# Performance work log

Measured on AMD Instinct MI355X. Metric: run time of the kernel, lower is better.

## Reference

```python
import jax, jax.numpy as jnp
import numpy as np

B, D = 16384, 1280      # batch, EfficientNet-b0 feature dim (model._fc.in_features)
C1, C2, C3 = 8, 6, 4    # fanout per tree level: 8 roots, 6 children each, 4 leaves each


def setup_inputs() -> dict:
    key = jax.random.key(0)
    ks = jax.random.split(key, 7)
    sc = 0.02
    x = jax.random.normal(ks[0], (B, D), dtype=jnp.float32)
    # root classifier: self.final = Linear(1280 -> n[0]=8)
    W_final = jax.random.normal(ks[1], (D, C1), dtype=jnp.float32) * sc
    b_final = jnp.zeros((C1,), dtype=jnp.float32)
    # level-1 node linears: Linear(1281 -> 6); split into feature part Wp and upper-scalar column wu
    Wp1 = jax.random.normal(ks[2], (C1, D, C2), dtype=jnp.float32) * sc
    wu1 = jax.random.normal(ks[3], (C1, C2), dtype=jnp.float32) * sc
    b1 = jnp.zeros((C1, C2), dtype=jnp.float32)
    # level-2 node linears: Linear(1281 -> 4)
    Wp2 = jax.random.normal(ks[4], (C1, C2, D, C3), dtype=jnp.float32) * sc
    wu2 = jax.random.normal(ks[5], (C1, C2, C3), dtype=jnp.float32) * sc
    b2 = jnp.zeros((C1, C2, C3), dtype=jnp.float32)
    return {"x": x, "W_final": W_final, "b_final": b_final,
            "Wp1": Wp1, "wu1": wu1, "b1": b1,
            "Wp2": Wp2, "wu2": wu2, "b2": b2}


def reference(x, W_final, b_final, Wp1, wu1, b1, Wp2, wu2, b2):
    # penultimate = x.clone().detach()
    pen = jax.lax.stop_gradient(x)                      # (B, D)
    # root: raw final-linear outputs (NO softmax at root in the torch code)
    u1 = x @ W_final + b_final                          # (B, C1) == upper for level-1 nodes
    # level-1 nodes: line = softmax(Linear([pen, upper_scalar]))
    # Linear([pen, u]) == pen @ Wp + u * wu + b  (batched over all 8 nodes in one GEMM)
    logits1 = jnp.einsum('bd,idc->bic', pen, Wp1) + u1[:, :, None] * wu1[None] + b1[None]
    p1 = jax.nn.softmax(logits1, axis=-1)               # (B, C1, C2)
    u2 = p1 * u1[:, :, None]                            # upper for level-2 nodes
    # level-2 nodes
    logits2 = jnp.einsum('bd,ijdc->bijc', pen, Wp2) + u2[..., None] * wu2[None] + b2[None]
    p2 = jax.nn.softmax(logits2, axis=-1)               # (B, C1, C2, C3)
    u3 = p2 * u2[..., None]                             # upper for leaf nodes
    # output: for each node (sorted by path length, then lexicographic path),
    # the last column of xdict[node] == upper[node]. Row-major reshape matches
    # the sorted key order for single-char labels.
    return jnp.concatenate([u1, u2.reshape(B, C1 * C2), u3.reshape(B, C1 * C2 * C3)], axis=1)
```

## Files before the change

kernel.cpp:

```cpp
#include <hip/hip_runtime.h>
#include <stdint.h>
#include <stddef.h>

#define D_FEAT 1280
#define N_PAD  256
#define N_OUT  248
#define BM     64
#define BK     64
#define K_ITERS 20
#define W_TILE_BYTES (N_PAD * BK * 2)

typedef float f32x4 __attribute__((ext_vector_type(4)));
typedef short s16x8 __attribute__((ext_vector_type(8)));
typedef unsigned int u32x4 __attribute__((ext_vector_type(4)));

__device__ __forceinline__ unsigned short f2bf(float f) {
  union { float f; unsigned int u; } v; v.f = f;
  unsigned int r = (v.u + 0x7fffu + ((v.u >> 16) & 1u)) >> 16;
  return (unsigned short)r;
}

__device__ __forceinline__ unsigned int cvt_pk(float a, float b) {
  unsigned int r;
  asm("v_cvt_pk_bf16_f32 %0, %1, %2" : "=v"(r) : "v"(a), "v"(b));
  return r;
}

__device__ __forceinline__ void gload16(const void* g, void* l) {
  __builtin_amdgcn_global_load_lds(
      (const __attribute__((address_space(1))) void*)g,
      (__attribute__((address_space(3))) void*)l, 16, 0, 0);
}

__global__ __launch_bounds__(256) void pack_w_kernel(
    const float* __restrict__ Wf, const float* __restrict__ Wp1,
    const float* __restrict__ Wp2, unsigned short* __restrict__ out) {
  int chunk = blockIdx.x * 256 + threadIdx.x;
  int s_phys = chunk & 7;
  int n = (chunk >> 3) & 255;
  int kt = chunk >> 11;
  int s_log = s_phys ^ (n & 7);
  int d0 = kt * BK + s_log * 8;
  float v[8];
#pragma unroll
  for (int e = 0; e < 8; ++e) v[e] = 0.0f;
  if (n < 8) {
#pragma unroll
    for (int e = 0; e < 8; ++e) v[e] = Wf[(d0 + e) * 8 + n];
  } else if (n < 56) {
    int m = n - 8;
    const float* base = Wp1 + (size_t)(m / 6) * D_FEAT * 6 + (m % 6);
#pragma unroll
    for (int e = 0; e < 8; ++e) v[e] = base[(d0 + e) * 6];
  } else if (n < 248) {
    int m = n - 56;
    const float* base = Wp2 + ((size_t)(m / 24) * 6 + ((m % 24) >> 2)) * D_FEAT * 4 + (m & 3);
#pragma unroll
    for (int e = 0; e < 8; ++e) v[e] = base[(d0 + e) * 4];
  }
  union { u32x4 u; s16x8 s; } pk;
#pragma unroll
  for (int h = 0; h < 4; ++h) pk.u[h] = cvt_pk(v[2 * h], v[2 * h + 1]);
  *(s16x8*)(out + (size_t)chunk * 8) = pk.s;
}

__global__ __launch_bounds__(512, 2) void tree_head_kernel(
    const float* __restrict__ x, const unsigned short* __restrict__ Wb,
    const float* __restrict__ b_final, const float* __restrict__ wu1,
    const float* __restrict__ b1, const float* __restrict__ wu2,
    const float* __restrict__ b2, float* __restrict__ out) {
  __shared__ __align__(16) char smem[122880];
  char* A0 = smem;
  char* A1 = smem + 8192;
  char* A2 = smem + 16384;
  char* B0 = smem + 24576;
  char* B1 = smem + 57344;
  char* B2 = smem + 90112;

  const int tid  = threadIdx.x;
  const int lane = tid & 63;
  const int wave = tid >> 6;
  const int wm   = wave >> 2;
  const int wn   = wave & 3;
  const int l15  = lane & 15;
  const int lh   = lane >> 4;
  const int row0 = blockIdx.x * BM;

  f32x4 acc[2][4];
#pragma unroll
  for (int m = 0; m < 2; ++m)
#pragma unroll
    for (int n = 0; n < 4; ++n)
#pragma unroll
      for (int j = 0; j < 4; ++j) acc[m][n][j] = 0.0f;

  const int arow = tid >> 3;
  const int aslot = tid & 7;
  const char* aptr = (const char*)x + ((size_t)(row0 + arow) * D_FEAT + aslot * 8) * 4;
  const int awoff = arow * 128 + ((aslot ^ (arow & 7)) << 4);
  const char* bsrc = (const char*)Wb + wave * 1024 + lane * 16;
  const int bdst = wave * 1024;

  f32x4 ra[3][2];

#define STAGEB(kt_, dB_) do {                                                 \
    _Pragma("unroll")                                                         \
    for (int j_ = 0; j_ < 4; ++j_)                                            \
      gload16(bsrc + (size_t)(kt_) * W_TILE_BYTES + j_ * 8192,                \
              (dB_) + bdst + j_ * 8192);                                      \
  } while (0)

#define LOADA(kt_, ri_) do {                                                  \
    ra[ri_][0] = *(const f32x4*)(aptr + (kt_) * 256);                         \
    ra[ri_][1] = *(const f32x4*)(aptr + (kt_) * 256 + 16);                    \
  } while (0)

#define WRITEA(ri_, dA_) do {                                                 \
    union { u32x4 u; s16x8 s; } pk_;                                          \
    pk_.u[0] = cvt_pk(ra[ri_][0][0], ra[ri_][0][1]);                          \
    pk_.u[1] = cvt_pk(ra[ri_][0][2], ra[ri_][0][3]);                          \
    pk_.u[2] = cvt_pk(ra[ri_][1][0], ra[ri_][1][1]);                          \
    pk_.u[3] = cvt_pk(ra[ri_][1][2], ra[ri_][1][3]);                          \
    *(s16x8*)((dA_) + awoff) = pk_.s;                                         \
  } while (0)

#define COMPUTE(cA_, cB_) do {                                                \
    s16x8 fr[2][2];                                                           \
    _Pragma("unroll")                                                         \
    for (int m_ = 0; m_ < 2; ++m_) {                                          \
      int rl_ = wm * 32 + m_ * 16 + l15;                                      \
      _Pragma("unroll")                                                       \
      for (int ks_ = 0; ks_ < 2; ++ks_) {                                     \
        int sl_ = ks_ * 4 + lh;                                               \
        fr[m_][ks_] = *(const s16x8*)((cA_) + rl_ * 128 +                     \
                                      ((sl_ ^ (rl_ & 7)) << 4));              \
      }                                                                       \
    }                                                                         \
    _Pragma("unroll")                                                         \
    for (int ks_ = 0; ks_ < 2; ++ks_) {                                       \
      int sl_ = ks_ * 4 + lh;                                                 \
      _Pragma("unroll")                                                       \
      for (int nf_ = 0; nf_ < 4; ++nf_) {                                     \
        int n_ = wn * 64 + nf_ * 16 + l15;                                    \
        s16x8 b_ = *(const s16x8*)((cB_) + n_ * 128 + ((sl_ ^ (n_ & 7)) << 4));\
        acc[0][nf_] = __builtin_amdgcn_mfma_f32_16x16x32_bf16(fr[0][ks_], b_, acc[0][nf_], 0, 0, 0); \
        acc[1][nf_] = __builtin_amdgcn_mfma_f32_16x16x32_bf16(fr[1][ks_], b_, acc[1][nf_], 0, 0, 0); \
      }                                                                       \
    }                                                                         \
  } while (0)

#define ITER(kt_, cA_, cB_, wA_, sB_, ls_, ws_) do {                          \
    asm volatile("s_waitcnt lgkmcnt(0)" ::: "memory");                        \
    __builtin_amdgcn_sched_barrier(0);                                        \
    __builtin_amdgcn_s_barrier();                                             \
    __builtin_amdgcn_sched_barrier(0);                                        \
    STAGEB((kt_) + 2, sB_);                                                   \
    LOADA((kt_) + 3, ls_);                                                    \
    __builtin_amdgcn_sched_barrier(0);                                        \
    asm volatile("s_waitcnt vmcnt(8)" ::: "memory");                          \
    __builtin_amdgcn_sched_barrier(0);                                        \
    WRITEA(ws_, wA_);                                                         \
    COMPUTE(cA_, cB_);                                                        \
  } while (0)

  STAGEB(0, B0);
  LOADA(0, 0);
  LOADA(1, 1);
  STAGEB(1, B1);
  LOADA(2, 2);
  __builtin_amdgcn_sched_barrier(0);
  asm volatile("s_waitcnt vmcnt(8)" ::: "memory");
  __builtin_amdgcn_sched_barrier(0);
  WRITEA(0, A0);

  for (int t = 0; t < 5; ++t) {
    ITER(3 * t + 0, A0, B0, A1, B2, 0, 1);
    ITER(3 * t + 1, A1, B1, A2, B0, 1, 2);
    ITER(3 * t + 2, A2, B2, A0, B1, 2, 0);
  }
  ITER(15, A0, B0, A1, B2, 0, 1);
  ITER(16, A1, B1, A2, B0, 1, 2);

  asm volatile("s_waitcnt lgkmcnt(0)" ::: "memory");
  __builtin_amdgcn_sched_barrier(0);
  __builtin_amdgcn_s_barrier();
  __builtin_amdgcn_sched_barrier(0);
  STAGEB(19, B1);
  __builtin_amdgcn_sched_barrier(0);
  asm volatile("s_waitcnt vmcnt(6)" ::: "memory");
  __builtin_amdgcn_sched_barrier(0);
  WRITEA(0, A0);
  COMPUTE(A2, B2);

  asm volatile("s_waitcnt lgkmcnt(0)" ::: "memory");
  __builtin_amdgcn_sched_barrier(0);
  __builtin_amdgcn_s_barrier();
  __builtin_amdgcn_sched_barrier(0);
  asm volatile("s_waitcnt vmcnt(0)" ::: "memory");
  __builtin_amdgcn_sched_barrier(0);
  WRITEA(1, A1);
  COMPUTE(A0, B0);

  asm volatile("s_waitcnt lgkmcnt(0)" ::: "memory");
  __builtin_amdgcn_sched_barrier(0);
  __builtin_amdgcn_s_barrier();
  __builtin_amdgcn_sched_barrier(0);
  COMPUTE(A1, B1);

  __syncthreads();

  float* Ls = (float*)smem;
#pragma unroll
  for (int m = 0; m < 2; ++m)
#pragma unroll
    for (int nf = 0; nf < 4; ++nf) {
      int col = wn * 64 + nf * 16 + l15;
      if (col < N_OUT) {
        int rbase = wm * 32 + m * 16 + (lh << 2);
#pragma unroll
        for (int i = 0; i < 4; ++i) Ls[col * 65 + rbase + i] = acc[m][nf][i];
      }
    }
  __syncthreads();

  const int p = tid & 7;
  const int r = tid >> 3;
  float* orow = out + (size_t)(row0 + r) * N_OUT;

  float ui = Ls[p * 65 + r] + b_final[p];
  orow[p] = ui;

  float lg[6];
  float mx = -1e30f;
#pragma unroll
  for (int c = 0; c < 6; ++c) {
    lg[c] = Ls[(8 + p * 6 + c) * 65 + r] + ui * wu1[p * 6 + c] + b1[p * 6 + c];
    mx = fmaxf(mx, lg[c]);
  }
  float s = 0.0f;
#pragma unroll
  for (int c = 0; c < 6; ++c) { lg[c] = __expf(lg[c] - mx); s += lg[c]; }
  float sc = ui / s;
  float u2v[6];
#pragma unroll
  for (int c = 0; c < 6; ++c) {
    u2v[c] = lg[c] * sc;
    orow[8 + p * 6 + c] = u2v[c];
  }

#pragma unroll
  for (int j = 0; j < 6; ++j) {
    int g = p * 6 + j;
    float ug = u2v[j];
    float l2[4];
    float m2 = -1e30f;
#pragma unroll
    for (int c = 0; c < 4; ++c) {
      l2[c] = Ls[(56 + g * 4 + c) * 65 + r] + ug * wu2[g * 4 + c] + b2[g * 4 + c];
      m2 = fmaxf(m2, l2[c]);
    }
    float s2 = 0.0f;
#pragma unroll
    for (int c = 0; c < 4; ++c) { l2[c] = __expf(l2[c] - m2); s2 += l2[c]; }
    float sc2 = ug / s2;
    f32x4 o;
#pragma unroll
    for (int c = 0; c < 4; ++c) o[c] = l2[c] * sc2;
    *(f32x4*)(orow + 56 + g * 4) = o;
  }
#undef STAGEB
#undef LOADA
#undef WRITEA
#undef COMPUTE
#undef ITER
}

extern "C" void kernel_launch(void* const* d_in, const int* in_sizes, int n_in,
                              void* d_out, int out_size, void* d_ws, size_t ws_size,
                              hipStream_t stream) {
  const float* x   = (const float*)d_in[0];
  const float* Wf  = (const float*)d_in[1];
  const float* bf  = (const float*)d_in[2];
  const float* Wp1 = (const float*)d_in[3];
  const float* wu1 = (const float*)d_in[4];
  const float* b1  = (const float*)d_in[5];
  const float* Wp2 = (const float*)d_in[6];
  const float* wu2 = (const float*)d_in[7];
  const float* b2  = (const float*)d_in[8];
  float* out = (float*)d_out;
  unsigned short* Wb = (unsigned short*)d_ws;

  pack_w_kernel<<<160, 256, 0, stream>>>(Wf, Wp1, Wp2, Wb);
  tree_head_kernel<<<16384 / BM, 512, 0, stream>>>(x, Wb, bf, wu1, b1, wu2, b2, out);
}
```

Baseline: 34.98 us.

## Halve row tile to 32 with 4-wave blocks and double-buffered LDS pipeline

Shrinks the per-block row tile from 64 to 32 rows and the block from 8 to 4 waves, so each wave now covers all 32 rows and a 64-column slice. The triple-buffered A/B LDS ring becomes double-buffered, with B staging issued one tile ahead instead of two. This cuts LDS from 120KB to 72KB and doubles the grid to 512 blocks, giving better CU coverage and occupancy. In exchange the shared bf16 weight tile is re-read from L2 twice as often per row, and the shallower prefetch leaves less latency hiding.

```diff
diff --git a/kernel.cpp b/kernel.cpp
--- a/kernel.cpp
+++ b/kernel.cpp
@@ -5,7 +5,7 @@
 #define D_FEAT 1280
 #define N_PAD  256
 #define N_OUT  248
-#define BM     64
+#define BM     32
 #define BK     64
 #define K_ITERS 20
 #define W_TILE_BYTES (N_PAD * BK * 2)
@@ -13,12 +13,6 @@
 typedef float f32x4 __attribute__((ext_vector_type(4)));
 typedef short s16x8 __attribute__((ext_vector_type(8)));
 typedef unsigned int u32x4 __attribute__((ext_vector_type(4)));
-
-__device__ __forceinline__ unsigned short f2bf(float f) {
-  union { float f; unsigned int u; } v; v.f = f;
-  unsigned int r = (v.u + 0x7fffu + ((v.u >> 16) & 1u)) >> 16;
-  return (unsigned short)r;
-}
 
 __device__ __forceinline__ unsigned int cvt_pk(float a, float b) {
   unsigned int r;
@@ -64,24 +58,20 @@
   *(s16x8*)(out + (size_t)chunk * 8) = pk.s;
 }
 
-__global__ __launch_bounds__(512, 2) void tree_head_kernel(
+__global__ __launch_bounds__(256, 2) void tree_head_kernel(
     const float* __restrict__ x, const unsigned short* __restrict__ Wb,
     const float* __restrict__ b_final, const float* __restrict__ wu1,
     const float* __restrict__ b1, const float* __restrict__ wu2,
     const float* __restrict__ b2, float* __restrict__ out) {
-  __shared__ __align__(16) char smem[122880];
-  char* A0 = smem;
-  char* A1 = smem + 8192;
-  char* A2 = smem + 16384;
-  char* B0 = smem + 24576;
-  char* B1 = smem + 57344;
-  char* B2 = smem + 90112;
+  __shared__ __align__(16) char smem[73728];
+  char* Ab0 = smem;
+  char* Ab1 = smem + 4096;
+  char* Bb0 = smem + 8192;
+  char* Bb1 = smem + 40960;
 
   const int tid  = threadIdx.x;
   const int lane = tid & 63;
   const int wave = tid >> 6;
-  const int wm   = wave >> 2;
-  const int wn   = wave & 3;
   const int l15  = lane & 15;
   const int lh   = lane >> 4;
   const int row0 = blockIdx.x * BM;
@@ -105,9 +95,9 @@
 
 #define STAGEB(kt_, dB_) do {                                                 \
     _Pragma("unroll")                                                         \
-    for (int j_ = 0; j_ < 4; ++j_)                                            \
-      gload16(bsrc + (size_t)(kt_) * W_TILE_BYTES + j_ * 8192,                \
-              (dB_) + bdst + j_ * 8192);                                      \
+    for (int j_ = 0; j_ < 8; ++j_)                                            \
+      gload16(bsrc + (size_t)(kt_) * W_TILE_BYTES + j_ * 4096,                \
+              (dB_) + bdst + j_ * 4096);                                      \
   } while (0)
 
 #define LOADA(kt_, ri_) do {                                                  \
@@ -128,7 +118,7 @@
     s16x8 fr[2][2];                                                           \
     _Pragma("unroll")                                                         \
     for (int m_ = 0; m_ < 2; ++m_) {                                          \
-      int rl_ = wm * 32 + m_ * 16 + l15;                                      \
+      int rl_ = m_ * 16 + l15;                                                \
       _Pragma("unroll")                                                       \
       for (int ks_ = 0; ks_ < 2; ++ks_) {                                     \
         int sl_ = ks_ * 4 + lh;                                               \
@@ -141,7 +131,7 @@
       int sl_ = ks_ * 4 + lh;                                                 \
       _Pragma("unroll")                                                       \
       for (int nf_ = 0; nf_ < 4; ++nf_) {                                     \
-        int n_ = wn * 64 + nf_ * 16 + l15;                                    \
+        int n_ = wave * 64 + nf_ * 16 + l15;                                  \
         s16x8 b_ = *(const s16x8*)((cB_) + n_ * 128 + ((sl_ ^ (n_ & 7)) << 4));\
         acc[0][nf_] = __builtin_amdgcn_mfma_f32_16x16x32_bf16(fr[0][ks_], b_, acc[0][nf_], 0, 0, 0); \
         acc[1][nf_] = __builtin_amdgcn_mfma_f32_16x16x32_bf16(fr[1][ks_], b_, acc[1][nf_], 0, 0, 0); \
@@ -149,63 +139,64 @@
     }                                                                         \
   } while (0)
 
-#define ITER(kt_, cA_, cB_, wA_, sB_, ls_, ws_) do {                          \
-    asm volatile("s_waitcnt lgkmcnt(0)" ::: "memory");                        \
+#define ITER(vm_, cA_, cB_, wA_, sB_, skt_, lakt_, ls_, ws_) do {             \
+    asm volatile("s_waitcnt vmcnt(" #vm_ ") lgkmcnt(0)" ::: "memory");        \
     __builtin_amdgcn_sched_barrier(0);                                        \
     __builtin_amdgcn_s_barrier();                                             \
     __builtin_amdgcn_sched_barrier(0);                                        \
-    STAGEB((kt_) + 2, sB_);                                                   \
-    LOADA((kt_) + 3, ls_);                                                    \
-    __builtin_amdgcn_sched_barrier(0);                                        \
-    asm volatile("s_waitcnt vmcnt(8)" ::: "memory");                          \
+    STAGEB(skt_, sB_);                                                        \
+    LOADA(lakt_, ls_);                                                        \
     __builtin_amdgcn_sched_barrier(0);                                        \
     WRITEA(ws_, wA_);                                                         \
     COMPUTE(cA_, cB_);                                                        \
   } while (0)
 
-  STAGEB(0, B0);
+  STAGEB(0, Bb0);
   LOADA(0, 0);
   LOADA(1, 1);
-  STAGEB(1, B1);
   LOADA(2, 2);
   __builtin_amdgcn_sched_barrier(0);
-  asm volatile("s_waitcnt vmcnt(8)" ::: "memory");
-  __builtin_amdgcn_sched_barrier(0);
-  WRITEA(0, A0);
-
-  for (int t = 0; t < 5; ++t) {
-    ITER(3 * t + 0, A0, B0, A1, B2, 0, 1);
-    ITER(3 * t + 1, A1, B1, A2, B0, 1, 2);
-    ITER(3 * t + 2, A2, B2, A0, B1, 2, 0);
-  }
-  ITER(15, A0, B0, A1, B2, 0, 1);
-  ITER(16, A1, B1, A2, B0, 1, 2);
-
-  asm volatile("s_waitcnt lgkmcnt(0)" ::: "memory");
+  asm volatile("s_waitcnt vmcnt(4)" ::: "memory");
+  __builtin_amdgcn_sched_barrier(0);
+  WRITEA(0, Ab0);
+
+  for (int t = 0; t < 2; ++t) {
+    ITER(2, Ab0, Bb0, Ab1, Bb1, 6 * t + 1, 6 * t + 3, 0, 1);
+    ITER(2, Ab1, Bb1, Ab0, Bb0, 6 * t + 2, 6 * t + 4, 1, 2);
+    ITER(2, Ab0, Bb0, Ab1, Bb1, 6 * t + 3, 6 * t + 5, 2, 0);
+    ITER(2, Ab1, Bb1, Ab0, Bb0, 6 * t + 4, 6 * t + 6, 0, 1);
+    ITER(2, Ab0, Bb0, Ab1, Bb1, 6 * t + 5, 6 * t + 7, 1, 2);
+    ITER(2, Ab1, Bb1, Ab0, Bb0, 6 * t + 6, 6 * t + 8, 2, 0);
+  }
+  ITER(2, Ab0, Bb0, Ab1, Bb1, 13, 15, 0, 1);
+  ITER(2, Ab1, Bb1, Ab0, Bb0, 14, 16, 1, 2);
+  ITER(2, Ab0, Bb0, Ab1, Bb1, 15, 17, 2, 0);
+  ITER(2, Ab1, Bb1, Ab0, Bb0, 16, 18, 0, 1);
+  ITER(2, Ab0, Bb0, Ab1, Bb1, 17, 19, 1, 2);
+
+  asm volatile("s_waitcnt vmcnt(2) lgkmcnt(0)" ::: "memory");
   __builtin_amdgcn_sched_barrier(0);
   __builtin_amdgcn_s_barrier();
   __builtin_amdgcn_sched_barrier(0);
-  STAGEB(19, B1);
-  __builtin_amdgcn_sched_barrier(0);
-  asm volatile("s_waitcnt vmcnt(6)" ::: "memory");
-  __builtin_amdgcn_sched_barrier(0);
-  WRITEA(0, A0);
-  COMPUTE(A2, B2);
-
-  asm volatile("s_waitcnt lgkmcnt(0)" ::: "memory");
+  STAGEB(18, Bb0);
+  __builtin_amdgcn_sched_barrier(0);
+  WRITEA(0, Ab0);
+  COMPUTE(Ab1, Bb1);
+
+  asm volatile("s_waitcnt vmcnt(0) lgkmcnt(0)" ::: "memory");
   __builtin_amdgcn_sched_barrier(0);
   __builtin_amdgcn_s_barrier();
   __builtin_amdgcn_sched_barrier(0);
-  asm volatile("s_waitcnt vmcnt(0)" ::: "memory");
-  __builtin_amdgcn_sched_barrier(0);
-  WRITEA(1, A1);
-  COMPUTE(A0, B0);
-
-  asm volatile("s_waitcnt lgkmcnt(0)" ::: "memory");
+  STAGEB(19, Bb1);
+  __builtin_amdgcn_sched_barrier(0);
+  WRITEA(1, Ab1);
+  COMPUTE(Ab0, Bb0);
+
+  asm volatile("s_waitcnt vmcnt(0) lgkmcnt(0)" ::: "memory");
   __builtin_amdgcn_sched_barrier(0);
   __builtin_amdgcn_s_barrier();
   __builtin_amdgcn_sched_barrier(0);
-  COMPUTE(A1, B1);
+  COMPUTE(Ab1, Bb1);
 
   __syncthreads();
 
@@ -214,11 +205,11 @@
   for (int m = 0; m < 2; ++m)
 #pragma unroll
     for (int nf = 0; nf < 4; ++nf) {
-      int col = wn * 64 + nf * 16 + l15;
+      int col = wave * 64 + nf * 16 + l15;
       if (col < N_OUT) {
-        int rbase = wm * 32 + m * 16 + (lh << 2);
-#pragma unroll
-        for (int i = 0; i < 4; ++i) Ls[col * 65 + rbase + i] = acc[m][nf][i];
+        int rbase = m * 16 + (lh << 2);
+#pragma unroll
+        for (int i = 0; i < 4; ++i) Ls[col * 33 + rbase + i] = acc[m][nf][i];
       }
     }
   __syncthreads();
@@ -227,14 +218,14 @@
   const int r = tid >> 3;
   float* orow = out + (size_t)(row0 + r) * N_OUT;
 
-  float ui = Ls[p * 65 + r] + b_final[p];
+  float ui = Ls[p * 33 + r] + b_final[p];
   orow[p] = ui;
 
   float lg[6];
   float mx = -1e30f;
 #pragma unroll
   for (int c = 0; c < 6; ++c) {
-    lg[c] = Ls[(8 + p * 6 + c) * 65 + r] + ui * wu1[p * 6 + c] + b1[p * 6 + c];
+    lg[c] = Ls[(8 + p * 6 + c) * 33 + r] + ui * wu1[p * 6 + c] + b1[p * 6 + c];
     mx = fmaxf(mx, lg[c]);
   }
   float s = 0.0f;
@@ -256,7 +247,7 @@
     float m2 = -1e30f;
 #pragma unroll
     for (int c = 0; c < 4; ++c) {
-      l2[c] = Ls[(56 + g * 4 + c) * 65 + r] + ug * wu2[g * 4 + c] + b2[g * 4 + c];
+      l2[c] = Ls[(56 + g * 4 + c) * 33 + r] + ug * wu2[g * 4 + c] + b2[g * 4 + c];
       m2 = fmaxf(m2, l2[c]);
     }
     float s2 = 0.0f;
@@ -291,5 +282,5 @@
   unsigned short* Wb = (unsigned short*)d_ws;
 
   pack_w_kernel<<<160, 256, 0, stream>>>(Wf, Wp1, Wp2, Wb);
-  tree_head_kernel<<<16384 / BM, 512, 0, stream>>>(x, Wb, bf, wu1, b1, wu2, b2, out);
-}
+  tree_head_kernel<<<16384 / BM, 256, 0, stream>>>(x, Wb, bf, wu1, b1, wu2, b2, out);
+}
```

New measurement: 37.92 us. +8.4%, slower.
